# Performance work log

Measured on AMD Instinct MI355X. Metric: run time of the kernel, lower is better.

## Reference

```python
import jax, jax.numpy as jnp
import numpy as np

D_MODEL = 1024
N_HEAD = 16
HEAD_SIZE = D_MODEL // N_HEAD


def setup_inputs() -> dict:
    key = jax.random.key(0)
    ks = jax.random.split(key, 7)
    B, T, E = 2, 2048, D_MODEL
    scale = 0.02
    return {
        "q": jax.random.normal(ks[0], (B, T, E), dtype=jnp.float32),
        "k": jax.random.normal(ks[1], (B, T, E), dtype=jnp.float32),
        "v": jax.random.normal(ks[2], (B, T, E), dtype=jnp.float32),
        "Wq": jax.random.normal(ks[3], (E, E), dtype=jnp.float32) * scale,
        "Wk": jax.random.normal(ks[4], (E, E), dtype=jnp.float32) * scale,
        "Wv": jax.random.normal(ks[5], (E, E), dtype=jnp.float32) * scale,
        "Wo": jax.random.normal(ks[6], (E, E), dtype=jnp.float32) * scale,
    }


def reference(q, k, v, Wq, Wk, Wv, Wo):
    B, T, E = q.shape
    # torch nn.Linear(bias=False): y = x @ W.T
    qh = (q @ Wq.T).reshape(B, T, N_HEAD, HEAD_SIZE).transpose(0, 2, 1, 3)  # [B,H,T,Dh]
    kh = (k @ Wk.T).reshape(B, T, N_HEAD, HEAD_SIZE).transpose(0, 2, 1, 3)
    vh = (v @ Wv.T).reshape(B, T, N_HEAD, HEAD_SIZE).transpose(0, 2, 1, 3)

    scale = 1.0 / jnp.sqrt(jnp.asarray(HEAD_SIZE, dtype=q.dtype))
    wei = jnp.einsum("bhqd,bhkd->bhqk", qh, kh) * scale  # [B,H,T,T]

    # causal mask (tril): positions j > i set to -inf
    causal = jnp.tril(jnp.ones((T, T), dtype=bool))
    wei = jnp.where(causal, wei, jnp.asarray(-jnp.inf, dtype=wei.dtype))

    attn = jax.nn.softmax(wei, axis=-1)
    out = jnp.einsum("bhqk,bhkd->bhqd", attn, vh)  # [B,H,T,Dh]
    out = out.transpose(0, 2, 1, 3).reshape(B, T, E)
    return out @ Wo.T  # dropout p=0.0 -> identity
```

## Files before the change

### kernel.cpp

```cpp
#include <hip/hip_runtime.h>
#include <hip/hip_bf16.h>
#include <cstddef>
#include <cstdint>

#define B_SZ   2
#define T_SEQ  2048
#define E_DIM  1024
#define N_HEAD 16
#define HEAD   64

typedef unsigned short u16;
typedef unsigned int u32;
using frag8 = __attribute__((ext_vector_type(8))) short;
using f32x4 = __attribute__((ext_vector_type(4))) float;

__device__ inline u16 f2bf(float x) {
    __hip_bfloat16 h = __float2bfloat16(x);
    return *reinterpret_cast<u16*>(&h);
}

__device__ inline u32 pack_bf16x2(float lo, float hi) {
    float2 t; t.x = lo; t.y = hi;
    __hip_bfloat162 p = __float22bfloat162_rn(t);
    return *reinterpret_cast<u32*>(&p);
}

__device__ inline void gl2lds16(const void* g, void* l) {
    auto gp = reinterpret_cast<const __attribute__((address_space(1))) unsigned int*>(
        reinterpret_cast<uintptr_t>(g));
    auto lp = reinterpret_cast<__attribute__((address_space(3))) unsigned int*>(
        reinterpret_cast<uintptr_t>(l));
    __builtin_amdgcn_global_load_lds(gp, lp, 16, 0, 0);
}

struct CastArgs {
    const float* src[7];
    u16* dst[7];
    int n[7];
    float scale[7];
};

__global__ __launch_bounds__(256) void cast_f32_bf16(CastArgs a) {
    const int t = blockIdx.y;
    const int i0 = (blockIdx.x * 256 + threadIdx.x) * 8;
    if (i0 >= a.n[t]) return;
    const float sc = a.scale[t];
    const float4 f0 = *(const float4*)(a.src[t] + i0);
    const float4 f1 = *(const float4*)(a.src[t] + i0 + 4);
    uint4 r;
    r.x = pack_bf16x2(f0.x * sc, f0.y * sc);
    r.y = pack_bf16x2(f0.z * sc, f0.w * sc);
    r.z = pack_bf16x2(f1.x * sc, f1.y * sc);
    r.w = pack_bf16x2(f1.z * sc, f1.w * sc);
    *(uint4*)(a.dst[t] + i0) = r;
}

__device__ inline void gemm_core(const u16* __restrict__ X,
                                 const u16* __restrict__ W,
                                 void* __restrict__ Yv, int mode,
                                 int bm0, int bn0) {
    __shared__ u16 As[2][64 * 64];
    __shared__ u16 Bs[2][128 * 64];

    const int tid = threadIdx.x;
    const int w = tid >> 6;
    const int lane = tid & 63;
    const int ln = lane & 15;
    const int quad = lane >> 4;
    const int wm = (w & 1) * 32;
    const int wn = (w >> 1) * 64;

    const int l8 = lane >> 3;
    const int g = (lane & 7) ^ l8;

    const u16* Ag = X + (size_t)(bm0 + w * 16 + l8) * 1024 + g * 8;
    const u16* Bg = W + (size_t)(bn0 + w * 32 + l8) * 1024 + g * 8;
    const int al = __builtin_amdgcn_readfirstlane(w * 1024);
    const int bl = __builtin_amdgcn_readfirstlane(w * 2048);

    const f32x4 zf = {0.f, 0.f, 0.f, 0.f};
    f32x4 acc[2][4];
#pragma unroll
    for (int mi = 0; mi < 2; ++mi)
#pragma unroll
        for (int nj = 0; nj < 4; ++nj) acc[mi][nj] = zf;

    const int sw = ln & 7;

    gl2lds16(Ag, &As[0][0] + al);
    gl2lds16(Ag + 8 * 1024, &As[0][0] + al + 512);
#pragma unroll
    for (int it = 0; it < 4; ++it)
        gl2lds16(Bg + (size_t)it * 8 * 1024, &Bs[0][0] + bl + it * 512);

    for (int k0 = 0; k0 < 1024; k0 += 64) {
        const int buf = (k0 >> 6) & 1;
        __syncthreads();

        if (k0 + 64 < 1024) {
            gl2lds16(Ag + k0 + 64, &As[buf ^ 1][0] + al);
            gl2lds16(Ag + 8 * 1024 + k0 + 64, &As[buf ^ 1][0] + al + 512);
#pragma unroll
            for (int it = 0; it < 4; ++it)
                gl2lds16(Bg + (size_t)it * 8 * 1024 + k0 + 64,
                         &Bs[buf ^ 1][0] + bl + it * 512);
        }

        frag8 a[2][2], b[4][2];
#pragma unroll
        for (int kc = 0; kc < 2; ++kc) {
            const int slot = ((kc * 4 + quad) ^ sw) * 8;
#pragma unroll
            for (int mi = 0; mi < 2; ++mi)
                a[mi][kc] = *(const frag8*)(&As[buf][0] + (wm + mi * 16 + ln) * 64 + slot);
#pragma unroll
            for (int nj = 0; nj < 4; ++nj)
                b[nj][kc] = *(const frag8*)(&Bs[buf][0] + (wn + nj * 16 + ln) * 64 + slot);
        }
#pragma unroll
        for (int kc = 0; kc < 2; ++kc)
#pragma unroll
            for (int mi = 0; mi < 2; ++mi)
#pragma unroll
                for (int nj = 0; nj < 4; ++nj)
                    acc[mi][nj] = __builtin_amdgcn_mfma_f32_16x16x32_bf16(
                        a[mi][kc], b[nj][kc], acc[mi][nj], 0, 0, 0);
    }

#pragma unroll
    for (int mi = 0; mi < 2; ++mi)
#pragma unroll
        for (int nj = 0; nj < 4; ++nj)
#pragma unroll
            for (int reg = 0; reg < 4; ++reg) {
                const int m = bm0 + wm + mi * 16 + quad * 4 + reg;
                const int n = bn0 + wn + nj * 16 + ln;
                if (mode == 1) {
                    ((float*)Yv)[(size_t)m * E_DIM + n] = acc[mi][nj][reg];
                } else {
                    const int b_ = m >> 11, t_ = m & (T_SEQ - 1);
                    const int h_ = n >> 6, d_ = n & (HEAD - 1);
                    const size_t idx = (mode == 0)
                        ? (((size_t)(b_ * N_HEAD + h_)) * T_SEQ + t_) * HEAD + d_
                        : (((size_t)(b_ * N_HEAD + h_)) * HEAD + d_) * T_SEQ + t_;
                    ((u16*)Yv)[idx] = f2bf(acc[mi][nj][reg]);
                }
            }
}

struct QkvArgs {
    const u16* X[3];
    const u16* W[3];
    u16* Y[3];
};

__global__ __launch_bounds__(256, 3) void gemm_qkv(QkvArgs a) {
    const int z = blockIdx.z;
    gemm_core(a.X[z], a.W[z], a.Y[z], z == 2 ? 2 : 0,
              blockIdx.x * 64, blockIdx.y * 128);
}

__global__ __launch_bounds__(256, 3) void gemm_out(const u16* __restrict__ X,
                                                   const u16* __restrict__ W,
                                                   float* __restrict__ Y) {
    gemm_core(X, W, Y, 1, blockIdx.x * 64, blockIdx.y * 128);
}

__global__ __launch_bounds__(512, 4) void attn_mfma(const u16* __restrict__ Qh,
                                                    const u16* __restrict__ Kh,
                                                    const u16* __restrict__ Vt_g,
                                                    u16* __restrict__ Aa) {
    __shared__ u16 Ks[2][128 * 64];
    __shared__ u16 Vs[2][64 * 128];

    const int tid = threadIdx.x;
    const int w = tid >> 6;
    const int wq = w & 3;
    const int wk = w >> 2;
    const int lane = tid & 63;
    const int ln = lane & 15;
    const int quad = lane >> 4;

    const int i = blockIdx.x;
    const int half = i >> 8;
    const int r_ = i & 255;
    const int bh = r_ >> 3;
    const int j = r_ & 7;
    const int qt = half ? j : (15 - j);
    const int q0 = qt * 128;
    const int qw = q0 + wq * 32;

    const size_t base = (size_t)bh * T_SEQ * HEAD;
    const u16* Qb = Qh + base;
    const u16* Kb = Kh + base;
    const u16* Vtb = Vt_g + base;

    const int l8 = lane >> 3;
    const int gk = (lane & 7) ^ l8;
    const int l16 = lane >> 4;
    const int c16 = lane & 15;
    const int sls = __builtin_amdgcn_readfirstlane(w * 1024);

    frag8 qf[2][2];
#pragma unroll
    for (int qq = 0; qq < 2; ++qq)
#pragma unroll
        for (int kc = 0; kc < 2; ++kc)
            qf[qq][kc] = *(const frag8*)(Qb + (size_t)(qw + qq * 16 + ln) * HEAD +
                                         kc * 32 + quad * 8);

    const f32x4 zf = {0.f, 0.f, 0.f, 0.f};
    f32x4 o[4][2];
    float rsl[2] = {0.f, 0.f};
#pragma unroll
    for (int dt = 0; dt < 4; ++dt)
#pragma unroll
        for (int qq = 0; qq < 2; ++qq) o[dt][qq] = zf;

    const int ktiles = qt + 1;

#pragma unroll
    for (int it = 0; it < 2; ++it) {
        const int krow = w * 16 + it * 8 + l8;
        gl2lds16(Kb + (size_t)krow * HEAD + gk * 8, &Ks[0][0] + sls + it * 512);
        const int vrow = w * 8 + it * 4 + l16;
        const int gv = c16 ^ (vrow & 7);
        gl2lds16(Vtb + (size_t)vrow * T_SEQ + gv * 8, &Vs[0][0] + sls + it * 512);
    }

    const int sw = ln & 7;
    const int hsel = quad >> 1;
    const int s_lo = ((quad & 1) * 2) * 16 + ln;
    const int s_hi = s_lo + 16;

    for (int kt = 0; kt < ktiles; ++kt) {
        const int k0 = kt << 7;
        const int buf = kt & 1;
        __syncthreads();

        if (kt + 1 < ktiles) {
            const int k1 = k0 + 128;
#pragma unroll
            for (int it = 0; it < 2; ++it) {
                const int krow = w * 16 + it * 8 + l8;
                gl2lds16(Kb + (size_t)(k1 + krow) * HEAD + gk * 8,
                         &Ks[buf ^ 1][0] + sls + it * 512);
                const int vrow = w * 8 + it * 4 + l16;
                const int gv = c16 ^ (vrow & 7);
                gl2lds16(Vtb + (size_t)vrow * T_SEQ + k1 + gv * 8,
                         &Vs[buf ^ 1][0] + sls + it * 512);
            }
        }

        const int kbase = k0 + wk * 64;
        if (kbase <= qw + 31) {
            const bool msk = (kbase + 63 > qw);
            u32 pk[4][2][2];
#pragma unroll
            for (int kk = 0; kk < 4; ++kk) {
                f32x4 st[2] = {zf, zf};
#pragma unroll
                for (int kc = 0; kc < 2; ++kc) {
                    const int slot = ((kc * 4 + quad) ^ sw) * 8;
                    const frag8 kf = *(const frag8*)(&Ks[buf][0] +
                                                     (wk * 64 + kk * 16 + ln) * 64 + slot);
                    st[0] = __builtin_amdgcn_mfma_f32_16x16x32_bf16(kf, qf[0][kc], st[0], 0, 0, 0);
                    st[1] = __builtin_amdgcn_mfma_f32_16x16x32_bf16(kf, qf[1][kc], st[1], 0, 0, 0);
                }
#pragma unroll
                for (int qq = 0; qq < 2; ++qq) {
                    float e[4];
#pragma unroll
                    for (int reg = 0; reg < 4; ++reg) {
                        const int key = kbase + kk * 16 + quad * 4 + reg;
                        const int qg = qw + qq * 16 + ln;
                        float ev = __expf(st[qq][reg]);
                        if (msk) ev = (key <= qg) ? ev : 0.f;
                        e[reg] = ev;
                        rsl[qq] += ev;
                    }
                    pk[kk][qq][0] = pack_bf16x2(e[0], e[1]);
                    pk[kk][qq][1] = pack_bf16x2(e[2], e[3]);
                }
            }

#pragma unroll
            for (int kc = 0; kc < 2; ++kc) {
                union { frag8 f; u32 d[4]; } pb[2];
#pragma unroll
                for (int qq = 0; qq < 2; ++qq) {
                    const u32 a00 = __shfl(pk[kc * 2][qq][0], s_lo, 64);
                    const u32 a01 = __shfl(pk[kc * 2][qq][1], s_lo, 64);
                    const u32 a02 = __shfl(pk[kc * 2][qq][0], s_hi, 64);
                    const u32 a03 = __shfl(pk[kc * 2][qq][1], s_hi, 64);
                    const u32 a10 = __shfl(pk[kc * 2 + 1][qq][0], s_lo, 64);
                    const u32 a11 = __shfl(pk[kc * 2 + 1][qq][1], s_lo, 64);
                    const u32 a12 = __shfl(pk[kc * 2 + 1][qq][0], s_hi, 64);
                    const u32 a13 = __shfl(pk[kc * 2 + 1][qq][1], s_hi, 64);
                    pb[qq].d[0] = hsel ? a10 : a00;
                    pb[qq].d[1] = hsel ? a11 : a01;
                    pb[qq].d[2] = hsel ? a12 : a02;
                    pb[qq].d[3] = hsel ? a13 : a03;
                }
                const int slotv = (((wk * 2 + kc) * 4 + quad) ^ sw) * 8;
#pragma unroll
                for (int dt = 0; dt < 4; ++dt) {
                    const frag8 vf = *(const frag8*)(&Vs[buf][0] + (dt * 16 + ln) * 128 + slotv);
                    o[dt][0] = __builtin_amdgcn_mfma_f32_16x16x32_bf16(vf, pb[0].f, o[dt][0], 0, 0, 0);
                    o[dt][1] = __builtin_amdgcn_mfma_f32_16x16x32_bf16(vf, pb[1].f, o[dt][1], 0, 0, 0);
                }
            }
        }
    }

#pragma unroll
    for (int qq = 0; qq < 2; ++qq) {
        rsl[qq] += __shfl_xor(rsl[qq], 16, 64);
        rsl[qq] += __shfl_xor(rsl[qq], 32, 64);
    }

    __syncthreads();
    float* ored = (float*)&Ks[0][0];
    float* lred = (float*)&Vs[0][0];
    if (wk == 1) {
#pragma unroll
        for (int dt = 0; dt < 4; ++dt)
#pragma unroll
            for (int qq = 0; qq < 2; ++qq)
#pragma unroll
                for (int rg = 0; rg < 4; ++rg)
                    ored[(dt * 8 + qq * 4 + rg) * 256 + wq * 64 + lane] = o[dt][qq][rg];
        lred[wq * 64 + lane] = rsl[0];
        lred[256 + wq * 64 + lane] = rsl[1];
    }
    __syncthreads();
    if (wk == 0) {
#pragma unroll
        for (int dt = 0; dt < 4; ++dt)
#pragma unroll
            for (int qq = 0; qq < 2; ++qq)
#pragma unroll
                for (int rg = 0; rg < 4; ++rg)
                    o[dt][qq][rg] += ored[(dt * 8 + qq * 4 + rg) * 256 + wq * 64 + lane];
        rsl[0] += lred[wq * 64 + lane];
        rsl[1] += lred[256 + wq * 64 + lane];

        const float inv0 = 1.f / rsl[0];
        const float inv1 = 1.f / rsl[1];
        const int b_ = bh >> 4, h_ = bh & (N_HEAD - 1);
#pragma unroll
        for (int qq = 0; qq < 2; ++qq) {
            const float inv = qq ? inv1 : inv0;
            const int qg = qw + qq * 16 + ln;
            u16* rowp = Aa + ((size_t)(b_ * T_SEQ + qg)) * E_DIM + h_ * HEAD;
#pragma unroll
            for (int dt = 0; dt < 4; ++dt)
#pragma unroll
                for (int rp = 0; rp < 2; ++rp) {
                    const u32 v = pack_bf16x2(o[dt][qq][2 * rp] * inv,
                                              o[dt][qq][2 * rp + 1] * inv);
                    *(u32*)(rowp + dt * 16 + quad * 4 + rp * 2) = v;
                }
        }
    }
}

extern "C" void kernel_launch(void* const* d_in, const int* in_sizes, int n_in,
                              void* d_out, int out_size, void* d_ws, size_t ws_size,
                              hipStream_t stream) {
    const float* q  = (const float*)d_in[0];
    const float* k  = (const float*)d_in[1];
    const float* v  = (const float*)d_in[2];
    const float* Wq = (const float*)d_in[3];
    const float* Wk = (const float*)d_in[4];
    const float* Wv = (const float*)d_in[5];
    const float* Wo = (const float*)d_in[6];

    u16* ws = (u16*)d_ws;
    const size_t M4 = (size_t)4 * 1024 * 1024;
    const size_t M1 = (size_t)1024 * 1024;
    u16* qb  = ws;
    u16* kb  = ws + M4;
    u16* vb  = ws + 2 * M4;
    u16* Wqb = ws + 3 * M4;
    u16* Wkb = ws + 3 * M4 + M1;
    u16* Wvb = ws + 3 * M4 + 2 * M1;
    u16* Wob = ws + 3 * M4 + 3 * M1;
    u16* Qh  = ws + 4 * M4;
    u16* Kh  = ws + 5 * M4;
    u16* Vht = ws + 6 * M4;
    u16* Aa  = ws + 7 * M4;

    CastArgs ca;
    ca.src[0] = q;  ca.src[1] = k;  ca.src[2] = v;
    ca.src[3] = Wq; ca.src[4] = Wk; ca.src[5] = Wv; ca.src[6] = Wo;
    ca.dst[0] = qb;  ca.dst[1] = kb;  ca.dst[2] = vb;
    ca.dst[3] = Wqb; ca.dst[4] = Wkb; ca.dst[5] = Wvb; ca.dst[6] = Wob;
    ca.n[0] = ca.n[1] = ca.n[2] = (int)M4;
    ca.n[3] = ca.n[4] = ca.n[5] = ca.n[6] = (int)M1;
    ca.scale[0] = ca.scale[1] = ca.scale[2] = 1.f;
    ca.scale[3] = 0.125f;
    ca.scale[4] = ca.scale[5] = ca.scale[6] = 1.f;
    cast_f32_bf16<<<dim3(2048, 7), 256, 0, stream>>>(ca);

    QkvArgs ga;
    ga.X[0] = qb;  ga.X[1] = kb;  ga.X[2] = vb;
    ga.W[0] = Wqb; ga.W[1] = Wkb; ga.W[2] = Wvb;
    ga.Y[0] = Qh;  ga.Y[1] = Kh;  ga.Y[2] = Vht;
    gemm_qkv<<<dim3(64, 8, 3), 256, 0, stream>>>(ga);

    attn_mfma<<<dim3(512), 512, 0, stream>>>(Qh, Kh, Vht, Aa);

    gemm_out<<<dim3(64, 8), 256, 0, stream>>>(Aa, Wob, (float*)d_out);
}
```

Baseline: 201.2 us.

## Halve attention tile sizes to 64 queries by 64 keys for more blocks

Shrinks the attention block's query tile from 128 to 64 rows and its key/value tile from 128 to 64. Each wave now handles 16 queries and 32 keys. The grid doubles to 1024 blocks, LDS per block halves, and the launch bound is raised to allow 8 blocks per CU, aiming for better occupancy and finer causal load balancing. In exchange there is less K/V reuse per block, twice the global K/V traffic, and more barriers per unit of work.

```diff
diff --git a/kernel.cpp b/kernel.cpp
--- a/kernel.cpp
+++ b/kernel.cpp
@@ -166,12 +166,12 @@
     gemm_core(X, W, Y, 1, blockIdx.x * 64, blockIdx.y * 128);
 }
 
-__global__ __launch_bounds__(512, 4) void attn_mfma(const u16* __restrict__ Qh,
+__global__ __launch_bounds__(512, 8) void attn_mfma(const u16* __restrict__ Qh,
                                                     const u16* __restrict__ Kh,
                                                     const u16* __restrict__ Vt_g,
                                                     u16* __restrict__ Aa) {
-    __shared__ u16 Ks[2][128 * 64];
-    __shared__ u16 Vs[2][64 * 128];
+    __shared__ u16 Ks[2][64 * 64];
+    __shared__ u16 Vs[2][64 * 64];
 
     const int tid = threadIdx.x;
     const int w = tid >> 6;
@@ -182,13 +182,13 @@
     const int quad = lane >> 4;
 
     const int i = blockIdx.x;
-    const int half = i >> 8;
-    const int r_ = i & 255;
-    const int bh = r_ >> 3;
-    const int j = r_ & 7;
-    const int qt = half ? j : (15 - j);
-    const int q0 = qt * 128;
-    const int qw = q0 + wq * 32;
+    const int half = i >> 9;
+    const int r_ = i & 511;
+    const int bh = r_ >> 4;
+    const int j = r_ & 15;
+    const int qt = half ? j : (31 - j);
+    const int q0 = qt * 64;
+    const int qw = q0 + wq * 16;
 
     const size_t base = (size_t)bh * T_SEQ * HEAD;
     const u16* Qb = Qh + base;
@@ -197,35 +197,25 @@
 
     const int l8 = lane >> 3;
     const int gk = (lane & 7) ^ l8;
-    const int l16 = lane >> 4;
-    const int c16 = lane & 15;
-    const int sls = __builtin_amdgcn_readfirstlane(w * 1024);
-
-    frag8 qf[2][2];
-#pragma unroll
-    for (int qq = 0; qq < 2; ++qq)
-#pragma unroll
-        for (int kc = 0; kc < 2; ++kc)
-            qf[qq][kc] = *(const frag8*)(Qb + (size_t)(qw + qq * 16 + ln) * HEAD +
-                                         kc * 32 + quad * 8);
+    const int sls = __builtin_amdgcn_readfirstlane(w * 512);
+
+    frag8 qf[2];
+#pragma unroll
+    for (int kc = 0; kc < 2; ++kc)
+        qf[kc] = *(const frag8*)(Qb + (size_t)(qw + ln) * HEAD + kc * 32 + quad * 8);
 
     const f32x4 zf = {0.f, 0.f, 0.f, 0.f};
-    f32x4 o[4][2];
-    float rsl[2] = {0.f, 0.f};
-#pragma unroll
-    for (int dt = 0; dt < 4; ++dt)
-#pragma unroll
-        for (int qq = 0; qq < 2; ++qq) o[dt][qq] = zf;
+    f32x4 o[4];
+    float rsl = 0.f;
+#pragma unroll
+    for (int dt = 0; dt < 4; ++dt) o[dt] = zf;
 
     const int ktiles = qt + 1;
 
-#pragma unroll
-    for (int it = 0; it < 2; ++it) {
-        const int krow = w * 16 + it * 8 + l8;
-        gl2lds16(Kb + (size_t)krow * HEAD + gk * 8, &Ks[0][0] + sls + it * 512);
-        const int vrow = w * 8 + it * 4 + l16;
-        const int gv = c16 ^ (vrow & 7);
-        gl2lds16(Vtb + (size_t)vrow * T_SEQ + gv * 8, &Vs[0][0] + sls + it * 512);
+    {
+        const int row = w * 8 + l8;
+        gl2lds16(Kb + (size_t)row * HEAD + gk * 8, &Ks[0][0] + sls);
+        gl2lds16(Vtb + (size_t)row * T_SEQ + gk * 8, &Vs[0][0] + sls);
     }
 
     const int sw = ln & 7;
@@ -234,90 +224,71 @@
     const int s_hi = s_lo + 16;
 
     for (int kt = 0; kt < ktiles; ++kt) {
-        const int k0 = kt << 7;
+        const int k0 = kt << 6;
         const int buf = kt & 1;
         __syncthreads();
 
         if (kt + 1 < ktiles) {
-            const int k1 = k0 + 128;
-#pragma unroll
-            for (int it = 0; it < 2; ++it) {
-                const int krow = w * 16 + it * 8 + l8;
-                gl2lds16(Kb + (size_t)(k1 + krow) * HEAD + gk * 8,
-                         &Ks[buf ^ 1][0] + sls + it * 512);
-                const int vrow = w * 8 + it * 4 + l16;
-                const int gv = c16 ^ (vrow & 7);
-                gl2lds16(Vtb + (size_t)vrow * T_SEQ + k1 + gv * 8,
-                         &Vs[buf ^ 1][0] + sls + it * 512);
-            }
+            const int k1 = k0 + 64;
+            const int row = w * 8 + l8;
+            gl2lds16(Kb + (size_t)(k1 + row) * HEAD + gk * 8, &Ks[buf ^ 1][0] + sls);
+            gl2lds16(Vtb + (size_t)row * T_SEQ + k1 + gk * 8, &Vs[buf ^ 1][0] + sls);
         }
 
-        const int kbase = k0 + wk * 64;
-        if (kbase <= qw + 31) {
-            const bool msk = (kbase + 63 > qw);
-            u32 pk[4][2][2];
-#pragma unroll
-            for (int kk = 0; kk < 4; ++kk) {
-                f32x4 st[2] = {zf, zf};
+        const int kbase = k0 + wk * 32;
+        if (kbase <= qw + 15) {
+            const bool msk = (kbase + 31 > qw);
+            u32 pk[2][2];
+#pragma unroll
+            for (int kk = 0; kk < 2; ++kk) {
+                f32x4 st = zf;
 #pragma unroll
                 for (int kc = 0; kc < 2; ++kc) {
                     const int slot = ((kc * 4 + quad) ^ sw) * 8;
                     const frag8 kf = *(const frag8*)(&Ks[buf][0] +
-                                                     (wk * 64 + kk * 16 + ln) * 64 + slot);
-                    st[0] = __builtin_amdgcn_mfma_f32_16x16x32_bf16(kf, qf[0][kc], st[0], 0, 0, 0);
-                    st[1] = __builtin_amdgcn_mfma_f32_16x16x32_bf16(kf, qf[1][kc], st[1], 0, 0, 0);
+                                                     (wk * 32 + kk * 16 + ln) * 64 + slot);
+                    st = __builtin_amdgcn_mfma_f32_16x16x32_bf16(kf, qf[kc], st, 0, 0, 0);
                 }
-#pragma unroll
-                for (int qq = 0; qq < 2; ++qq) {
-                    float e[4];
-#pragma unroll
-                    for (int reg = 0; reg < 4; ++reg) {
-                        const int key = kbase + kk * 16 + quad * 4 + reg;
-                        const int qg = qw + qq * 16 + ln;
-                        float ev = __expf(st[qq][reg]);
-                        if (msk) ev = (key <= qg) ? ev : 0.f;
-                        e[reg] = ev;
-                        rsl[qq] += ev;
-                    }
-                    pk[kk][qq][0] = pack_bf16x2(e[0], e[1]);
-                    pk[kk][qq][1] = pack_bf16x2(e[2], e[3]);
+                float e[4];
+#pragma unroll
+                for (int reg = 0; reg < 4; ++reg) {
+                    const int key = kbase + kk * 16 + quad * 4 + reg;
+                    const int qg = qw + ln;
+                    float ev = __expf(st[reg]);
+                    if (msk) ev = (key <= qg) ? ev : 0.f;
+                    e[reg] = ev;
+                    rsl += ev;
                 }
-            }
-
-#pragma unroll
-            for (int kc = 0; kc < 2; ++kc) {
-                union { frag8 f; u32 d[4]; } pb[2];
-#pragma unroll
-                for (int qq = 0; qq < 2; ++qq) {
-                    const u32 a00 = __shfl(pk[kc * 2][qq][0], s_lo, 64);
-                    const u32 a01 = __shfl(pk[kc * 2][qq][1], s_lo, 64);
-                    const u32 a02 = __shfl(pk[kc * 2][qq][0], s_hi, 64);
-                    const u32 a03 = __shfl(pk[kc * 2][qq][1], s_hi, 64);
-                    const u32 a10 = __shfl(pk[kc * 2 + 1][qq][0], s_lo, 64);
-                    const u32 a11 = __shfl(pk[kc * 2 + 1][qq][1], s_lo, 64);
-                    const u32 a12 = __shfl(pk[kc * 2 + 1][qq][0], s_hi, 64);
-                    const u32 a13 = __shfl(pk[kc * 2 + 1][qq][1], s_hi, 64);
-                    pb[qq].d[0] = hsel ? a10 : a00;
-                    pb[qq].d[1] = hsel ? a11 : a01;
-                    pb[qq].d[2] = hsel ? a12 : a02;
-                    pb[qq].d[3] = hsel ? a13 : a03;
-                }
-                const int slotv = (((wk * 2 + kc) * 4 + quad) ^ sw) * 8;
-#pragma unroll
-                for (int dt = 0; dt < 4; ++dt) {
-                    const frag8 vf = *(const frag8*)(&Vs[buf][0] + (dt * 16 + ln) * 128 + slotv);
-                    o[dt][0] = __builtin_amdgcn_mfma_f32_16x16x32_bf16(vf, pb[0].f, o[dt][0], 0, 0, 0);
-                    o[dt][1] = __builtin_amdgcn_mfma_f32_16x16x32_bf16(vf, pb[1].f, o[dt][1], 0, 0, 0);
-                }
+                pk[kk][0] = pack_bf16x2(e[0], e[1]);
+                pk[kk][1] = pack_bf16x2(e[2], e[3]);
+            }
+
+            union { frag8 f; u32 d[4]; } pb;
+            {
+                const u32 a00 = __shfl(pk[0][0], s_lo, 64);
+                const u32 a01 = __shfl(pk[0][1], s_lo, 64);
+                const u32 a02 = __shfl(pk[0][0], s_hi, 64);
+                const u32 a03 = __shfl(pk[0][1], s_hi, 64);
+                const u32 a10 = __shfl(pk[1][0], s_lo, 64);
+                const u32 a11 = __shfl(pk[1][1], s_lo, 64);
+                const u32 a12 = __shfl(pk[1][0], s_hi, 64);
+                const u32 a13 = __shfl(pk[1][1], s_hi, 64);
+                pb.d[0] = hsel ? a10 : a00;
+                pb.d[1] = hsel ? a11 : a01;
+                pb.d[2] = hsel ? a12 : a02;
+                pb.d[3] = hsel ? a13 : a03;
+            }
+            const int slotv = ((wk * 4 + quad) ^ sw) * 8;
+#pragma unroll
+            for (int dt = 0; dt < 4; ++dt) {
+                const frag8 vf = *(const frag8*)(&Vs[buf][0] + (dt * 16 + ln) * 64 + slotv);
+                o[dt] = __builtin_amdgcn_mfma_f32_16x16x32_bf16(vf, pb.f, o[dt], 0, 0, 0);
             }
         }
     }
 
-#pragma unroll
-    for (int qq = 0; qq < 2; ++qq) {
-        rsl[qq] += __shfl_xor(rsl[qq], 16, 64);
-        rsl[qq] += __shfl_xor(rsl[qq], 32, 64);
-    }
+    rsl += __shfl_xor(rsl, 16, 64);
+    rsl += __shfl_xor(rsl, 32, 64);
 
     __syncthreads();
     float* ored = (float*)&Ks[0][0];
@@ -326,42 +297,31 @@
 #pragma unroll
         for (int dt = 0; dt < 4; ++dt)
 #pragma unroll
-            for (int qq = 0; qq < 2; ++qq)
-#pragma unroll
-                for (int rg = 0; rg < 4; ++rg)
-                    ored[(dt * 8 + qq * 4 + rg) * 256 + wq * 64 + lane] = o[dt][qq][rg];
-        lred[wq * 64 + lane] = rsl[0];
-        lred[256 + wq * 64 + lane] = rsl[1];
+            for (int rg = 0; rg < 4; ++rg)
+                ored[(dt * 4 + rg) * 256 + wq * 64 + lane] = o[dt][rg];
+        lred[wq * 64 + lane] = rsl;
     }
     __syncthreads();
     if (wk == 0) {
 #pragma unroll
         for (int dt = 0; dt < 4; ++dt)
 #pragma unroll
-            for (int qq = 0; qq < 2; ++qq)
-#pragma unroll
-                for (int rg = 0; rg < 4; ++rg)
-                    o[dt][qq][rg] += ored[(dt * 8 + qq * 4 + rg) * 256 + wq * 64 + lane];
-        rsl[0] += lred[wq * 64 + lane];
-        rsl[1] += lred[256 + wq * 64 + lane];
-
-        const float inv0 = 1.f / rsl[0];
-        const float inv1 = 1.f / rsl[1];
+            for (int rg = 0; rg < 4; ++rg)
+                o[dt][rg] += ored[(dt * 4 + rg) * 256 + wq * 64 + lane];
+        rsl += lred[wq * 64 + lane];
+
+        const float inv = 1.f / rsl;
         const int b_ = bh >> 4, h_ = bh & (N_HEAD - 1);
-#pragma unroll
-        for (int qq = 0; qq < 2; ++qq) {
-            const float inv = qq ? inv1 : inv0;
-            const int qg = qw + qq * 16 + ln;
-            u16* rowp = Aa + ((size_t)(b_ * T_SEQ + qg)) * E_DIM + h_ * HEAD;
-#pragma unroll
-            for (int dt = 0; dt < 4; ++dt)
-#pragma unroll
-                for (int rp = 0; rp < 2; ++rp) {
-                    const u32 v = pack_bf16x2(o[dt][qq][2 * rp] * inv,
-                                              o[dt][qq][2 * rp + 1] * inv);
-                    *(u32*)(rowp + dt * 16 + quad * 4 + rp * 2) = v;
-                }
-        }
+        const int qg = qw + ln;
+        u16* rowp = Aa + ((size_t)(b_ * T_SEQ + qg)) * E_DIM + h_ * HEAD;
+#pragma unroll
+        for (int dt = 0; dt < 4; ++dt)
+#pragma unroll
+            for (int rp = 0; rp < 2; ++rp) {
+                const u32 v = pack_bf16x2(o[dt][2 * rp] * inv,
+                                          o[dt][2 * rp + 1] * inv);
+                *(u32*)(rowp + dt * 16 + quad * 4 + rp * 2) = v;
+            }
     }
 }
 
@@ -409,7 +369,7 @@
     ga.Y[0] = Qh;  ga.Y[1] = Kh;  ga.Y[2] = Vht;
     gemm_qkv<<<dim3(64, 8, 3), 256, 0, stream>>>(ga);
 
-    attn_mfma<<<dim3(512), 512, 0, stream>>>(Qh, Kh, Vht, Aa);
+    attn_mfma<<<dim3(1024), 512, 0, stream>>>(Qh, Kh, Vht, Aa);
 
     gemm_out<<<dim3(64, 8), 256, 0, stream>>>(Aa, Wob, (float*)d_out);
 }
```

Result: no change. 202.9 us (+0.8%).
